# Kernel optimization log

Measured on AMD Instinct MI355X. Metric: run time of the kernel, lower is better.

## Reference

```python
import jax, jax.numpy as jnp
import numpy as np
from jax import lax

F1, D, F2 = 8, 2, 16
CTX = 64           # context = 1.0 s * 64 Hz
NCH = 64           # EEG channels
POOL1, POOL2 = 2, 5
BN_EPS = 1e-5


def _conv2d(x, w, b, padding, groups=1):
    y = lax.conv_general_dilated(x, w, (1, 1), padding,
                                 dimension_numbers=('NCHW', 'OIHW', 'NCHW'),
                                 feature_group_count=groups)
    return y + b[None, :, None, None]


def _bn(x, g, b, m, v):
    scale = g / jnp.sqrt(v + BN_EPS)
    return (x - m[None, :, None, None]) * scale[None, :, None, None] + b[None, :, None, None]


def _avgpool_w(x, k):
    y = lax.reduce_window(x, jnp.float32(0), lax.add, (1, 1, 1, k), (1, 1, 1, k), 'VALID')
    return y / k


def setup_inputs() -> dict:
    key = jax.random.key(0)
    ks = jax.random.split(key, 24)
    B, C, eegL = 16, NCH, 256
    f32 = jnp.float32
    inp = {
        'eeg': jax.random.normal(ks[0], (B, C, eegL), f32),
        'env': jax.random.normal(ks[1], (B, 2, eegL), f32),
        # conv1: Conv2d(1, F1, (1,3), padding='same')
        'conv1_w': jax.random.normal(ks[2], (F1, 1, 1, 3), f32) * 0.3,
        'conv1_b': jax.random.normal(ks[3], (F1,), f32) * 0.05,
        'bn1_g': jax.random.uniform(ks[4], (F1,), f32, 0.8, 1.2),
        'bn1_b': jax.random.normal(ks[5], (F1,), f32) * 0.05,
        'bn1_m': jax.random.normal(ks[6], (F1,), f32) * 0.1,
        'bn1_v': jax.random.uniform(ks[7], (F1,), f32, 0.5, 1.5),
        # conv2: Conv2d(F1, F1*D, (NCH,1), 'valid', groups=F1)
        'conv2_w': jax.random.normal(ks[8], (F1 * D, 1, NCH, 1), f32) * 0.05,
        'conv2_b': jax.random.normal(ks[9], (F1 * D,), f32) * 0.05,
        'bn2_g': jax.random.uniform(ks[10], (F1 * D,), f32, 0.8, 1.2),
        'bn2_b': jax.random.normal(ks[11], (F1 * D,), f32) * 0.05,
        'bn2_m': jax.random.normal(ks[12], (F1 * D,), f32) * 0.1,
        'bn2_v': jax.random.uniform(ks[13], (F1 * D,), f32, 0.5, 1.5),
        # conv3: depthwise Conv2d(F1*D, F1*D, (1,3), 'same', groups=F1*D)
        'conv3_w': jax.random.normal(ks[14], (F1 * D, 1, 1, 3), f32) * 0.3,
        'conv3_b': jax.random.normal(ks[15], (F1 * D,), f32) * 0.05,
        # conv4: pointwise Conv2d(F1*D, F2, (1,1))
        'conv4_w': jax.random.normal(ks[16], (F2, F1 * D, 1, 1), f32) * 0.2,
        'conv4_b': jax.random.normal(ks[17], (F2,), f32) * 0.05,
        'bn3_g': jax.random.uniform(ks[18], (F2,), f32, 0.8, 1.2),
        'bn3_b': jax.random.normal(ks[19], (F2,), f32) * 0.05,
        'bn3_m': jax.random.normal(ks[20], (F2,), f32) * 0.1,
        'bn3_v': jax.random.uniform(ks[21], (F2,), f32, 0.5, 1.5),
        # linear: F2 * (CTX // (POOL1*POOL2)) -> 1
        'lin_w': jax.random.normal(ks[22], (1, F2 * (CTX // (POOL1 * POOL2))), f32) * 0.1,
        'lin_b': jax.random.normal(ks[23], (1,), f32) * 0.05,
    }
    return inp


def _forward(eeg, conv1_w, conv1_b, bn1_g, bn1_b, bn1_m, bn1_v,
             conv2_w, conv2_b, bn2_g, bn2_b, bn2_m, bn2_v,
             conv3_w, conv3_b, conv4_w, conv4_b,
             bn3_g, bn3_b, bn3_m, bn3_v, lin_w, lin_b):
    B, C, eegL = eeg.shape
    L = eegL - CTX + 1
    # extract all overlapping windows: [B, C, L, CTX] -> [B*L, 1, C, CTX]
    idx = jnp.arange(L)[:, None] + jnp.arange(CTX)[None, :]
    win = eeg[:, :, idx]                      # [B, C, L, CTX]
    x = win.transpose(0, 2, 1, 3).reshape(B * L, 1, C, CTX)
    x = _conv2d(x, conv1_w, conv1_b, ((0, 0), (1, 1)))            # same pad on time
    x = _bn(x, bn1_g, bn1_b, bn1_m, bn1_v)
    x = _conv2d(x, conv2_w, conv2_b, ((0, 0), (0, 0)), groups=F1)  # spatial conv -> H=1
    x = _bn(x, bn2_g, bn2_b, bn2_m, bn2_v)
    x = jax.nn.elu(x)
    x = _avgpool_w(x, POOL1)
    x = _conv2d(x, conv3_w, conv3_b, ((0, 0), (1, 1)), groups=F1 * D)  # depthwise temporal
    x = _conv2d(x, conv4_w, conv4_b, ((0, 0), (0, 0)))                 # pointwise
    x = _bn(x, bn3_g, bn3_b, bn3_m, bn3_v)
    x = jax.nn.elu(x)
    x = _avgpool_w(x, POOL2)
    x = x.reshape(B * L, -1)                  # [B*L, F2*6]
    y = x @ lin_w.T + lin_b                   # [B*L, 1]
    return y.reshape(B, L)


def reference(eeg, env, conv1_w, conv1_b, bn1_g, bn1_b, bn1_m, bn1_v,
              conv2_w, conv2_b, bn2_g, bn2_b, bn2_m, bn2_v,
              conv3_w, conv3_b, conv4_w, conv4_b,
              bn3_g, bn3_b, bn3_m, bn3_v, lin_w, lin_b):
    assert env.shape[1] == 2  # n_streams check (env unused by the math)
    return _forward(eeg, conv1_w, conv1_b, bn1_g, bn1_b, bn1_m, bn1_v,
                    conv2_w, conv2_b, bn2_g, bn2_b, bn2_m, bn2_v,
                    conv3_w, conv3_b, conv4_w, conv4_b,
                    bn3_g, bn3_b, bn3_m, bn3_v, lin_w, lin_b)
```

## Files before the change

### kernel.cpp

```cpp
#include <hip/hip_runtime.h>
#include <math.h>

#define BN_EPS 1e-5f
#define LWIN   193
#define WPB    16
#define NBL    13
#define SLOC   96
#define STR    97

__device__ __forceinline__ float elu(float x) { return x > 0.f ? x : expm1f(x); }

__global__ __launch_bounds__(256) void eegnet_fused(
    const float* __restrict__ eeg,
    const float* __restrict__ c1w, const float* __restrict__ c1b,
    const float* __restrict__ bn1g, const float* __restrict__ bn1b,
    const float* __restrict__ bn1m, const float* __restrict__ bn1v,
    const float* __restrict__ w2,  const float* __restrict__ c2b,
    const float* __restrict__ bn2g, const float* __restrict__ bn2b,
    const float* __restrict__ bn2m, const float* __restrict__ bn2v,
    const float* __restrict__ c3w, const float* __restrict__ c3b,
    const float* __restrict__ c4w, const float* __restrict__ c4b,
    const float* __restrict__ bn3g, const float* __restrict__ bn3b,
    const float* __restrict__ bn3m, const float* __restrict__ bn3v,
    const float* __restrict__ linw, const float* __restrict__ linb,
    float* __restrict__ out)
{
    const int b   = blockIdx.x;
    const int L0  = blockIdx.y * WPB;
    const int g0  = L0 - 3;
    const int tid = threadIdx.x;
    const int lane16 = tid & 15;
    const int grp16  = tid >> 4;

    __shared__ float Eg[64][SLOC];
    __shared__ float Ul[16][STR];
    __shared__ float El[16][STR];
    __shared__ float P2[16][STR];
    __shared__ float Ql[16][STR];
    __shared__ float Ef[16][STR];
    __shared__ float S5[16][STR];
    __shared__ float w2t[64 * 16];
    __shared__ float cs[512];
    __shared__ float q0s[16][17], q1s[16][17];

    {
        const int wv = tid >> 6, ln = tid & 63;
        const float* ebase = eeg + b * 64 * 256;
        for (int c = wv; c < 64; c += 4) {
            int s1 = g0 + ln;       s1 = s1 < 0 ? 0 : (s1 > 255 ? 255 : s1);
            Eg[c][ln] = ebase[c * 256 + s1];
            if (ln < SLOC - 64) {
                int s2 = g0 + 64 + ln; s2 = s2 < 0 ? 0 : (s2 > 255 ? 255 : s2);
                Eg[c][64 + ln] = ebase[c * 256 + s2];
            }
        }
        for (int idx = tid; idx < 1024; idx += 256) {
            const int c = idx >> 4, o = idx & 15;
            w2t[idx] = w2[o * 64 + c];
        }
    }

    if (tid < 16) {
        const int f = tid, g = f >> 1;
        const float s1 = bn1g[g] / sqrtf(bn1v[g] + BN_EPS);
        const float o1 = bn1b[g] - bn1m[g] * s1;
        const float s2 = bn2g[f] / sqrtf(bn2v[f] + BN_EPS);
        const float o2 = bn2b[f] - bn2m[f] * s2;
        const float ss = s2 * s1;
        float S2 = 0.f;
        for (int c = 0; c < 64; ++c) S2 += w2[f * 64 + c];
        cs[      f] = ss * c1w[g * 3 + 0];
        cs[ 16 + f] = ss * c1w[g * 3 + 1];
        cs[ 32 + f] = ss * c1w[g * 3 + 2];
        cs[ 48 + f] = s2 * (fmaf(s1, c1b[g], o1) * S2 + c2b[f]) + o2;
        cs[ 64 + f] = c3w[f * 3 + 0];
        cs[ 80 + f] = c3w[f * 3 + 1];
        cs[ 96 + f] = c3w[f * 3 + 2];
        cs[112 + f] = c3b[f];
        const float s3 = bn3g[f] / sqrtf(bn3v[f] + BN_EPS);
        const float o3 = bn3b[f] - bn3m[f] * s3;
        cs[128 + f] = fmaf(s3, c4b[f], o3);
        #pragma unroll
        for (int o = 0; o < 16; ++o)
            cs[144 + o * 16 + f] = s3 * c4w[f * 16 + o];
    }
    if (tid >= 64 && tid < 160) cs[400 + tid - 64] = linw[tid - 64];
    if (tid == 160)             cs[496] = linb[0];
    __syncthreads();

    {
        float acc[6] = {0.f, 0.f, 0.f, 0.f, 0.f, 0.f};
        for (int c = 0; c < 64; ++c) {
            const float w = w2t[c * 16 + lane16];
            #pragma unroll
            for (int k = 0; k < 6; ++k)
                acc[k] = fmaf(w, Eg[c][grp16 + 16 * k], acc[k]);
        }
        #pragma unroll
        for (int k = 0; k < 6; ++k)
            Ul[lane16][grp16 + 16 * k] = acc[k];
    }
    __syncthreads();

    #pragma unroll
    for (int k = 0; k < 6; ++k) {
        const int i = grp16 + 16 * k, sg = g0 + i, o = lane16;
        const float um = (sg >= 1)   ? Ul[o][i > 0 ? i - 1 : 0] : 0.f;
        const float uc = Ul[o][i];
        const float up = (sg <= 254) ? Ul[o][i < SLOC - 1 ? i + 1 : SLOC - 1] : 0.f;
        El[o][i] = elu(fmaf(cs[o], um, fmaf(cs[16 + o], uc, fmaf(cs[32 + o], up, cs[48 + o]))));
    }
    __syncthreads();

    #pragma unroll
    for (int k = 0; k < 6; ++k) {
        const int i = grp16 + 16 * k, o = lane16;
        const int ip = i < SLOC - 1 ? i + 1 : SLOC - 1;
        P2[o][i] = 0.5f * (El[o][i] + El[o][ip]);
    }
    __syncthreads();

    #pragma unroll
    for (int k = 0; k < 6; ++k) {
        const int i = grp16 + 16 * k, o = lane16;
        const int im = i >= 2 ? i - 2 : 0;
        const int ip = i < SLOC - 2 ? i + 2 : SLOC - 1;
        Ql[o][i] = fmaf(cs[64 + o], P2[o][im],
                   fmaf(cs[80 + o], P2[o][i],
                   fmaf(cs[96 + o], P2[o][ip], cs[112 + o])));
    }
    __syncthreads();

    #pragma unroll
    for (int k = 0; k < 6; ++k) {
        const int i = grp16 + 16 * k, f = lane16;
        float r = cs[128 + f];
        #pragma unroll
        for (int o = 0; o < 16; ++o)
            r = fmaf(cs[144 + o * 16 + f], Ql[o][i], r);
        Ef[f][i] = elu(r);
    }
    __syncthreads();

    #pragma unroll
    for (int k = 0; k < 6; ++k) {
        const int i = grp16 + 16 * k, f = lane16;
        const int i2 = i + 2 < SLOC ? i + 2 : SLOC - 1;
        const int i4 = i + 4 < SLOC ? i + 4 : SLOC - 1;
        const int i6 = i + 6 < SLOC ? i + 6 : SLOC - 1;
        const int i8 = i + 8 < SLOC ? i + 8 : SLOC - 1;
        S5[f][i] = Ef[f][i] + Ef[f][i2] + Ef[f][i4] + Ef[f][i6] + Ef[f][i8];
    }
    __syncthreads();

    {
        const int w = grp16, o = lane16, l = L0 + w;
        if (l < LWIN) {
            const int li = w + 3;
            const float z0 = fmaf(cs[16 + o], Ul[o][li], fmaf(cs[32 + o], Ul[o][li + 1], cs[48 + o]));
            const float P0 = 0.5f * (elu(z0) + El[o][li + 1]);
            const float pa = P2[o][li + 2], pb = P2[o][li + 4];
            q0s[w][o] = fmaf(cs[80 + o], P0, fmaf(cs[96 + o], pa, cs[112 + o]));
            q1s[w][o] = fmaf(cs[64 + o], P0, fmaf(cs[80 + o], pa, fmaf(cs[96 + o], pb, cs[112 + o])));
        }
    }
    __syncthreads();

    {
        const int w = grp16, f = lane16, l = L0 + w;
        float part = 0.f;
        if (l < LWIN) {
            const int li = w + 3;
            float r0 = cs[128 + f], r1 = r0;
            #pragma unroll
            for (int o = 0; o < 16; ++o) {
                const float wt = cs[144 + o * 16 + f];
                r0 = fmaf(wt, q0s[w][o], r0);
                r1 = fmaf(wt, q1s[w][o], r1);
            }
            part = cs[400 + f * 6] * (elu(r0) + elu(r1) - Ef[f][li] - Ef[f][li + 2]);
            #pragma unroll
            for (int g = 0; g < 6; ++g)
                part = fmaf(cs[400 + f * 6 + g], S5[f][li + 10 * g], part);
        }
        part += __shfl_xor(part, 1);
        part += __shfl_xor(part, 2);
        part += __shfl_xor(part, 4);
        part += __shfl_xor(part, 8);
        if (f == 0 && l < LWIN) out[b * LWIN + l] = fmaf(0.2f, part, cs[496]);
    }
}

extern "C" void kernel_launch(void* const* d_in, const int* in_sizes, int n_in,
                              void* d_out, int out_size, void* d_ws, size_t ws_size,
                              hipStream_t stream) {
    const float* eeg  = (const float*)d_in[0];
    const float* c1w  = (const float*)d_in[2];
    const float* c1b  = (const float*)d_in[3];
    const float* bn1g = (const float*)d_in[4];
    const float* bn1b = (const float*)d_in[5];
    const float* bn1m = (const float*)d_in[6];
    const float* bn1v = (const float*)d_in[7];
    const float* w2   = (const float*)d_in[8];
    const float* c2b  = (const float*)d_in[9];
    const float* bn2g = (const float*)d_in[10];
    const float* bn2b = (const float*)d_in[11];
    const float* bn2m = (const float*)d_in[12];
    const float* bn2v = (const float*)d_in[13];
    const float* c3w  = (const float*)d_in[14];
    const float* c3b  = (const float*)d_in[15];
    const float* c4w  = (const float*)d_in[16];
    const float* c4b  = (const float*)d_in[17];
    const float* bn3g = (const float*)d_in[18];
    const float* bn3b = (const float*)d_in[19];
    const float* bn3m = (const float*)d_in[20];
    const float* bn3v = (const float*)d_in[21];
    const float* linw = (const float*)d_in[22];
    const float* linb = (const float*)d_in[23];

    eegnet_fused<<<dim3(16, NBL), 256, 0, stream>>>(
        eeg, c1w, c1b, bn1g, bn1b, bn1m, bn1v, w2, c2b,
        bn2g, bn2b, bn2m, bn2v, c3w, c3b, c4w, c4b,
        bn3g, bn3b, bn3m, bn3v, linw, linb, (float*)d_out);
}
```

Baseline: 18.15 us.

## Load EEG tile via direct global-to-LDS copies and retile spatial conv

Replaces the per-element EEG staging loop with 16-byte global_load_lds transfers into a flat LDS buffer, falling back to clamped scalar loads only at the signal edges. The spatial channel-reduction is retiled so each thread handles 4 output filters for one or two time positions, reading weights as float4. The parameter-folding prologue is also spread over more threads. The aim is lower load latency and fewer LDS reads per FMA, at the cost of branch divergence in the matmul (half the lanes do double work) and reliance on an AMD-specific intrinsic.

New measurement: 15.58 us (median of 2 runs). 14.1% less time.

```diff
diff --git a/kernel.cpp b/kernel.cpp
--- a/kernel.cpp
+++ b/kernel.cpp
@@ -7,6 +7,9 @@
 #define NBL    13
 #define SLOC   96
 #define STR    97
+
+typedef __attribute__((address_space(1))) const unsigned int gl_u32;
+typedef __attribute__((address_space(3))) unsigned int lds_u32;
 
 __device__ __forceinline__ float elu(float x) { return x > 0.f ? x : expm1f(x); }
 
@@ -32,73 +35,114 @@
     const int lane16 = tid & 15;
     const int grp16  = tid >> 4;
 
-    __shared__ float Eg[64][SLOC];
-    __shared__ float Ul[16][STR];
-    __shared__ float El[16][STR];
-    __shared__ float P2[16][STR];
-    __shared__ float Ql[16][STR];
-    __shared__ float Ef[16][STR];
-    __shared__ float S5[16][STR];
-    __shared__ float w2t[64 * 16];
-    __shared__ float cs[512];
-    __shared__ float q0s[16][17], q1s[16][17];
+    __shared__ __align__(16) float Eg[64 * SLOC];
+    __shared__ float4 w2t4[64 * 4];
+    __shared__ float  Ul[16][STR];
+    __shared__ float  El[16][STR];
+    __shared__ float  P2[16][STR];
+    __shared__ float  Ql[16][STR];
+    __shared__ float  Ef[16][STR];
+    __shared__ float  S5[16][STR];
+    __shared__ float  cs[512];
+    __shared__ float  q0s[16][17], q1s[16][17];
+
+    const float* ebase = eeg + b * 64 * 256;
 
     {
         const int wv = tid >> 6, ln = tid & 63;
-        const float* ebase = eeg + b * 64 * 256;
-        for (int c = wv; c < 64; c += 4) {
-            int s1 = g0 + ln;       s1 = s1 < 0 ? 0 : (s1 > 255 ? 255 : s1);
-            Eg[c][ln] = ebase[c * 256 + s1];
-            if (ln < SLOC - 64) {
-                int s2 = g0 + 64 + ln; s2 = s2 < 0 ? 0 : (s2 > 255 ? 255 : s2);
-                Eg[c][64 + ln] = ebase[c * 256 + s2];
+        #pragma unroll
+        for (int j = 0; j < 6; ++j) {
+            const int n    = wv * 6 + j;
+            const int fidx = n * 256 + ln * 4;
+            const int c    = fidx / SLOC;
+            const int i    = fidx - c * SLOC;
+            const int s    = g0 + i;
+            if (s >= 0 && s <= 252) {
+                __builtin_amdgcn_global_load_lds((gl_u32*)(ebase + c * 256 + s),
+                                                 (lds_u32*)&Eg[n * 256], 16, 0, 0);
+            } else {
+                const float* row = ebase + c * 256;
+                const int e0 = s     < 0 ? 0 : (s     > 255 ? 255 : s);
+                const int e1 = s + 1 < 0 ? 0 : (s + 1 > 255 ? 255 : s + 1);
+                const int e2 = s + 2 < 0 ? 0 : (s + 2 > 255 ? 255 : s + 2);
+                const int e3 = s + 3 < 0 ? 0 : (s + 3 > 255 ? 255 : s + 3);
+                *reinterpret_cast<float4*>(&Eg[fidx]) =
+                    make_float4(row[e0], row[e1], row[e2], row[e3]);
             }
         }
-        for (int idx = tid; idx < 1024; idx += 256) {
-            const int c = idx >> 4, o = idx & 15;
-            w2t[idx] = w2[o * 64 + c];
-        }
-    }
-
-    if (tid < 16) {
-        const int f = tid, g = f >> 1;
-        const float s1 = bn1g[g] / sqrtf(bn1v[g] + BN_EPS);
-        const float o1 = bn1b[g] - bn1m[g] * s1;
-        const float s2 = bn2g[f] / sqrtf(bn2v[f] + BN_EPS);
-        const float o2 = bn2b[f] - bn2m[f] * s2;
-        const float ss = s2 * s1;
-        float S2 = 0.f;
-        for (int c = 0; c < 64; ++c) S2 += w2[f * 64 + c];
-        cs[      f] = ss * c1w[g * 3 + 0];
-        cs[ 16 + f] = ss * c1w[g * 3 + 1];
-        cs[ 32 + f] = ss * c1w[g * 3 + 2];
-        cs[ 48 + f] = s2 * (fmaf(s1, c1b[g], o1) * S2 + c2b[f]) + o2;
-        cs[ 64 + f] = c3w[f * 3 + 0];
-        cs[ 80 + f] = c3w[f * 3 + 1];
-        cs[ 96 + f] = c3w[f * 3 + 2];
-        cs[112 + f] = c3b[f];
+    }
+
+    {
+        const int og = tid >> 6, c = tid & 63, o0 = og * 4;
+        w2t4[c * 4 + og] = make_float4(w2[(o0    ) * 64 + c], w2[(o0 + 1) * 64 + c],
+                                       w2[(o0 + 2) * 64 + c], w2[(o0 + 3) * 64 + c]);
+    }
+
+    if (tid < 64) {
+        const int f = tid & 15, q = tid >> 4;
+        float s2p = 0.f;
+        #pragma unroll
+        for (int k = 0; k < 16; ++k) s2p += w2[f * 64 + q * 16 + k];
+        s2p += __shfl_xor(s2p, 16);
+        s2p += __shfl_xor(s2p, 32);
+        if (tid < 16) {
+            const int g = f >> 1;
+            const float s1 = bn1g[g] / sqrtf(bn1v[g] + BN_EPS);
+            const float o1 = bn1b[g] - bn1m[g] * s1;
+            const float s2 = bn2g[f] / sqrtf(bn2v[f] + BN_EPS);
+            const float o2 = bn2b[f] - bn2m[f] * s2;
+            const float ss = s2 * s1;
+            cs[      f] = ss * c1w[g * 3 + 0];
+            cs[ 16 + f] = ss * c1w[g * 3 + 1];
+            cs[ 32 + f] = ss * c1w[g * 3 + 2];
+            cs[ 48 + f] = s2 * (fmaf(s1, c1b[g], o1) * s2p + c2b[f]) + o2;
+            cs[ 64 + f] = c3w[f * 3 + 0];
+            cs[ 80 + f] = c3w[f * 3 + 1];
+            cs[ 96 + f] = c3w[f * 3 + 2];
+            cs[112 + f] = c3b[f];
+        }
+    } else if (tid < 128) {
+        const int j = tid - 64, f = j & 15, quad = j >> 4;
         const float s3 = bn3g[f] / sqrtf(bn3v[f] + BN_EPS);
-        const float o3 = bn3b[f] - bn3m[f] * s3;
-        cs[128 + f] = fmaf(s3, c4b[f], o3);
-        #pragma unroll
-        for (int o = 0; o < 16; ++o)
+        if (quad == 0)
+            cs[128 + f] = fmaf(s3, c4b[f], bn3b[f] - bn3m[f] * s3);
+        #pragma unroll
+        for (int k = 0; k < 4; ++k) {
+            const int o = quad * 4 + k;
             cs[144 + o * 16 + f] = s3 * c4w[f * 16 + o];
-    }
-    if (tid >= 64 && tid < 160) cs[400 + tid - 64] = linw[tid - 64];
-    if (tid == 160)             cs[496] = linb[0];
-    __syncthreads();
-
-    {
-        float acc[6] = {0.f, 0.f, 0.f, 0.f, 0.f, 0.f};
+        }
+    } else if (tid < 224) {
+        cs[400 + tid - 128] = linw[tid - 128];
+    } else if (tid == 224) {
+        cs[496] = linb[0];
+    }
+    __syncthreads();
+
+    {
+        const int p  = tid & 63;
+        const int og = tid >> 6;
+        const bool two = (p < 32);
+        float a0 = 0.f, a1 = 0.f, a2 = 0.f, a3 = 0.f;
+        float b0 = 0.f, b1 = 0.f, b2 = 0.f, b3 = 0.f;
+        #pragma unroll 8
         for (int c = 0; c < 64; ++c) {
-            const float w = w2t[c * 16 + lane16];
-            #pragma unroll
-            for (int k = 0; k < 6; ++k)
-                acc[k] = fmaf(w, Eg[c][grp16 + 16 * k], acc[k]);
-        }
-        #pragma unroll
-        for (int k = 0; k < 6; ++k)
-            Ul[lane16][grp16 + 16 * k] = acc[k];
+            const float4 w = w2t4[c * 4 + og];
+            const float  e = Eg[c * SLOC + p];
+            a0 = fmaf(w.x, e, a0); a1 = fmaf(w.y, e, a1);
+            a2 = fmaf(w.z, e, a2); a3 = fmaf(w.w, e, a3);
+            if (two) {
+                const float e2 = Eg[c * SLOC + p + 64];
+                b0 = fmaf(w.x, e2, b0); b1 = fmaf(w.y, e2, b1);
+                b2 = fmaf(w.z, e2, b2); b3 = fmaf(w.w, e2, b3);
+            }
+        }
+        const int o0 = og * 4;
+        Ul[o0    ][p] = a0; Ul[o0 + 1][p] = a1;
+        Ul[o0 + 2][p] = a2; Ul[o0 + 3][p] = a3;
+        if (two) {
+            Ul[o0    ][p + 64] = b0; Ul[o0 + 1][p + 64] = b1;
+            Ul[o0 + 2][p + 64] = b2; Ul[o0 + 3][p + 64] = b3;
+        }
     }
     __syncthreads();
 
```
